# Performance work log

Measured on AMD Instinct MI355X. Metric: run time of the kernel, lower is better.

The kernel has to match this reference:

```python
import jax, jax.numpy as jnp
import numpy as np

N = 10000       # nodes
E = 320000      # edges (before self-loops)
IN = 128
HID = 256
OUT = 256
HEADS = 4
C = HID // HEADS  # 64 per-head channels
NEG_SLOPE = 0.2   # PyG GATConv default
BN_EPS = 1e-5


def setup_inputs() -> dict:
    key = jax.random.key(0)
    ks = jax.random.split(key, 24)
    x = jax.random.normal(ks[0], (N, IN), jnp.float32)
    edge_index = jax.random.randint(ks[1], (2, E), 0, N, dtype=jnp.int64)

    def glorot(k, shape, fan_in):
        return jax.random.normal(k, shape, jnp.float32) * (1.0 / np.sqrt(fan_in))

    inp = {"x": x, "edge_index": edge_index}
    # layer 0: IN -> HEADS x C (concat)
    inp["W0"] = glorot(ks[2], (IN, HEADS * C), IN)
    inp["as0"] = glorot(ks[3], (HEADS, C), C)
    inp["ad0"] = glorot(ks[4], (HEADS, C), C)
    inp["b0"] = jnp.zeros((HEADS * C,), jnp.float32)
    inp["g0"] = jnp.ones((HID,), jnp.float32)
    inp["be0"] = jnp.zeros((HID,), jnp.float32)
    # layer 1: HID -> HEADS x C (concat)
    inp["W1"] = glorot(ks[5], (HID, HEADS * C), HID)
    inp["as1"] = glorot(ks[6], (HEADS, C), C)
    inp["ad1"] = glorot(ks[7], (HEADS, C), C)
    inp["b1"] = jnp.zeros((HEADS * C,), jnp.float32)
    inp["g1"] = jnp.ones((HID,), jnp.float32)
    inp["be1"] = jnp.zeros((HID,), jnp.float32)
    # layer 2: HID -> OUT, heads=1, concat=False
    inp["W2"] = glorot(ks[8], (HID, OUT), HID)
    inp["as2"] = glorot(ks[9], (1, OUT), OUT)
    inp["ad2"] = glorot(ks[10], (1, OUT), OUT)
    inp["b2"] = jnp.zeros((OUT,), jnp.float32)
    inp["g2"] = jnp.ones((OUT,), jnp.float32)
    inp["be2"] = jnp.zeros((OUT,), jnp.float32)
    return inp


def gat_conv(x, src, dst, W, att_src, att_dst, bias, concat):
    """PyG GATConv (add_self_loops already applied to src/dst)."""
    H, Ch = att_src.shape
    h = (x @ W).reshape(-1, H, Ch)                      # [N, H, C]
    a_src = jnp.einsum('nhc,hc->nh', h, att_src)        # [N, H]
    a_dst = jnp.einsum('nhc,hc->nh', h, att_dst)
    alpha = jax.nn.leaky_relu(a_src[src] + a_dst[dst], NEG_SLOPE)  # [E', H]
    # segment softmax over incoming edges of each dst node
    amax = jax.ops.segment_max(alpha, dst, num_segments=N)
    alpha = jnp.exp(alpha - amax[dst])
    denom = jax.ops.segment_sum(alpha, dst, num_segments=N)
    alpha = alpha / (denom[dst] + 1e-16)
    msg = h[src] * alpha[:, :, None]                    # [E', H, C]
    out = jax.ops.segment_sum(msg, dst, num_segments=N) # [N, H, C]
    out = out.reshape(N, H * Ch) if concat else out.mean(axis=1)
    return out + bias


def batch_norm(x, gamma, beta):
    # training-mode BatchNorm1d over node dim (biased variance, eps=1e-5)
    m = x.mean(axis=0)
    v = jnp.mean((x - m) ** 2, axis=0)
    return (x - m) * jax.lax.rsqrt(v + BN_EPS) * gamma + beta


def reference(x, edge_index,
              W0, as0, ad0, b0, g0, be0,
              W1, as1, ad1, b1, g1, be1,
              W2, as2, ad2, b2, g2, be2):
    loop = jnp.arange(N, dtype=edge_index.dtype)
    src = jnp.concatenate([edge_index[0], loop])
    dst = jnp.concatenate([edge_index[1], loop])

    h = gat_conv(x, src, dst, W0, as0, ad0, b0, concat=True)
    h = jax.nn.relu(batch_norm(h, g0, be0))  # dropout inactive in eval
    h = gat_conv(h, src, dst, W1, as1, ad1, b1, concat=True)
    h = jax.nn.relu(batch_norm(h, g1, be1))
    h = gat_conv(h, src, dst, W2, as2, ad2, b2, concat=False)
    h = batch_norm(h, g2, be2)
    return h
```

## Files before the change

### kernel.cpp

```cpp
#include <hip/hip_runtime.h>
#include <math.h>

#define NN 10000
#define EE 320000
#define ET (EE + NN)

typedef __attribute__((ext_vector_type(8))) short short8;
typedef __attribute__((ext_vector_type(4))) float f32x4;
typedef unsigned short u16;

static __device__ __forceinline__ float b2f(u16 u) {
  return __uint_as_float(((unsigned)u) << 16);
}
static __device__ __forceinline__ u16 f2b(float f) {
  unsigned u = __float_as_uint(f);
  unsigned r = (u + 0x7FFFu + ((u >> 16) & 1u)) >> 16;
  return (u16)r;
}

__global__ void k_count(const int* __restrict__ ei, int* __restrict__ cnt) {
  int e = blockIdx.x * 256 + threadIdx.x;
  if (e < EE) atomicAdd(&cnt[ei[EE + e]], 1);
}

__global__ __launch_bounds__(1024) void k_scan(const int* __restrict__ cnt,
                                               int* __restrict__ rowst,
                                               int* __restrict__ cursor,
                                               int* __restrict__ csrc) {
  __shared__ int ws[16];
  int tid = threadIdx.x, lane = tid & 63, wv = tid >> 6;
  int base = tid * 10;
  int v[10];
  int tot = 0;
#pragma unroll
  for (int i = 0; i < 10; i++) {
    int idx = base + i;
    v[i] = (idx < NN) ? (cnt[idx] + 1) : 0;
    tot += v[i];
  }
  int sc = tot;
#pragma unroll
  for (int off = 1; off < 64; off <<= 1) {
    int t = __shfl_up(sc, off);
    if (lane >= off) sc += t;
  }
  if (lane == 63) ws[wv] = sc;
  __syncthreads();
  if (wv == 0 && lane < 16) {
    int val = ws[lane];
    int s = val;
#pragma unroll
    for (int off = 1; off < 16; off <<= 1) {
      int t = __shfl_up(s, off);
      if (lane >= off) s += t;
    }
    ws[lane] = s - val;
  }
  __syncthreads();
  int run = ws[wv] + sc - tot;
#pragma unroll
  for (int i = 0; i < 10; i++) {
    int idx = base + i;
    if (idx < NN) {
      rowst[idx] = run;
      csrc[run] = idx;
      cursor[idx] = run + 1;
      run += v[i];
    }
  }
  if (tid == 1023) rowst[NN] = run;
}

__global__ void k_fill(const int* __restrict__ ei, int* __restrict__ cursor,
                       int* __restrict__ csrc) {
  int e = blockIdx.x * 256 + threadIdx.x;
  if (e < EE) {
    int d = ei[EE + e];
    int pos = atomicAdd(&cursor[d], 1);
    csrc[pos] = ei[e];
  }
}

__global__ void k_casts(const float* __restrict__ x, const float* __restrict__ W0,
                        const float* __restrict__ W1, const float* __restrict__ W2,
                        u16* __restrict__ abf, u16* __restrict__ Wt0,
                        u16* __restrict__ Wt1, u16* __restrict__ Wt2) {
  int t = blockIdx.x * 256 + threadIdx.x;
  const int NX4 = NN * 128 / 4;
  if (t < NX4) {
    float4 f = ((const float4*)x)[t];
    ushort4 o;
    o.x = f2b(f.x); o.y = f2b(f.y); o.z = f2b(f.z); o.w = f2b(f.w);
    ((ushort4*)abf)[t] = o;
    return;
  }
  int u = t - NX4;
  if (u < 128 * 256) {
    int nI = u / 128, k = u - nI * 128;
    Wt0[u] = f2b(W0[(size_t)k * 256 + nI]);
    return;
  }
  u -= 128 * 256;
  if (u < 256 * 256) {
    int nI = u / 256, k = u - nI * 256;
    Wt1[u] = f2b(W1[(size_t)k * 256 + nI]);
    return;
  }
  u -= 256 * 256;
  if (u < 256 * 256) {
    int nI = u / 256, k = u - nI * 256;
    Wt2[u] = f2b(W2[(size_t)k * 256 + nI]);
  }
}

template <int KK, int BN>
__global__ __launch_bounds__(256) void k_gemm(
    const u16* __restrict__ A, const float* __restrict__ Af,
    const float* __restrict__ bkt, const float* __restrict__ gam,
    const float* __restrict__ bet, const u16* __restrict__ Wt,
    const float* __restrict__ as, const float* __restrict__ ad,
    u16* __restrict__ hb, float* __restrict__ asrc, float* __restrict__ adst,
    int H) {
  __shared__ float2 bnp[256];
  if (BN) {
    int t = threadIdx.x;
    float s = 0.f, q = 0.f;
#pragma unroll 8
    for (int b = 0; b < 32; b++) {
      s += bkt[b * 512 + t];
      q += bkt[b * 512 + 256 + t];
    }
    float m = s * (1.0f / NN);
    float v = q * (1.0f / NN) - m * m;
    float rs = rsqrtf(v + 1e-5f) * gam[t];
    bnp[t] = make_float2(rs, bet[t] - m * rs);
    __syncthreads();
  }
  int wv = threadIdx.x >> 6, lane = threadIdx.x & 63;
  int row0 = blockIdx.x * 64 + wv * 16;
  int col0 = blockIdx.y * 128;
  int r = lane & 15, g = lane >> 4;
  f32x4 acc[8];
#pragma unroll
  for (int nt = 0; nt < 8; nt++) acc[nt] = (f32x4){0.f, 0.f, 0.f, 0.f};

  int ar = row0 + r;
  if (ar > NN - 1) ar = NN - 1;

#pragma unroll
  for (int ks = 0; ks < KK / 32; ks++) {
    short8 af;
    if (BN == 0) {
      af = *(const short8*)(A + (size_t)ar * KK + ks * 32 + g * 8);
    } else {
      int c0 = ks * 32 + g * 8;
      float4 a0 = ((const float4*)Af)[(size_t)ar * (KK / 4) + c0 / 4];
      float4 a1 = ((const float4*)Af)[(size_t)ar * (KK / 4) + c0 / 4 + 1];
      float vv[8] = {a0.x, a0.y, a0.z, a0.w, a1.x, a1.y, a1.z, a1.w};
#pragma unroll
      for (int j = 0; j < 8; j++) {
        float2 p = bnp[c0 + j];
        float t = fmaxf(fmaf(vv[j], p.x, p.y), 0.f);
        af[j] = (short)f2b(t);
      }
    }
#pragma unroll
    for (int nt = 0; nt < 8; nt++) {
      short8 bf = *(const short8*)(Wt + (size_t)(col0 + nt * 16 + r) * KK + ks * 32 + g * 8);
      acc[nt] = __builtin_amdgcn_mfma_f32_16x16x32_bf16(af, bf, acc[nt], 0, 0, 0);
    }
  }
#pragma unroll
  for (int nt = 0; nt < 8; nt++) {
    int col = col0 + nt * 16 + r;
#pragma unroll
    for (int q = 0; q < 4; q++) {
      int row = row0 + g * 4 + q;
      if (row < NN) hb[(size_t)row * 256 + col] = f2b(acc[nt][q]);
    }
  }
  float asv[8], adv[8];
#pragma unroll
  for (int nt = 0; nt < 8; nt++) {
    asv[nt] = as[col0 + nt * 16 + r];
    adv[nt] = ad[col0 + nt * 16 + r];
  }
#pragma unroll
  for (int q = 0; q < 4; q++) {
    int row = row0 + g * 4 + q;
    if (H == 4) {
#pragma unroll
      for (int hh = 0; hh < 2; hh++) {
        float ps = 0.f, pd = 0.f;
#pragma unroll
        for (int k = 0; k < 4; k++) {
          ps = fmaf(acc[hh * 4 + k][q], asv[hh * 4 + k], ps);
          pd = fmaf(acc[hh * 4 + k][q], adv[hh * 4 + k], pd);
        }
#pragma unroll
        for (int off = 1; off < 16; off <<= 1) {
          ps += __shfl_xor(ps, off);
          pd += __shfl_xor(pd, off);
        }
        if (r == 0 && row < NN) {
          int slot = 2 * blockIdx.y + hh;
          asrc[row * 4 + slot] = ps;
          adst[row * 4 + slot] = pd;
        }
      }
    } else {
      float ps = 0.f, pd = 0.f;
#pragma unroll
      for (int nt = 0; nt < 8; nt++) {
        ps = fmaf(acc[nt][q], asv[nt], ps);
        pd = fmaf(acc[nt][q], adv[nt], pd);
      }
#pragma unroll
      for (int off = 1; off < 16; off <<= 1) {
        ps += __shfl_xor(ps, off);
        pd += __shfl_xor(pd, off);
      }
      if (r == 0 && row < NN) {
        int slot = 2 * blockIdx.y;
        asrc[row * 4 + slot] = ps;
        asrc[row * 4 + slot + 1] = 0.f;
        adst[row * 4 + slot] = pd;
        adst[row * 4 + slot + 1] = 0.f;
      }
    }
  }
}

template <int H>
__global__ __launch_bounds__(256) void k_softagg(
    const int* __restrict__ rowst, const int* __restrict__ csrc,
    const float* __restrict__ asrc, const float* __restrict__ adst,
    const u16* __restrict__ hb, const float* __restrict__ bias,
    float* __restrict__ out, float* __restrict__ bkt) {
  __shared__ int lds_s[4][128];
  __shared__ float lds_w[4][128][H];
  __shared__ float4 lds_rv[4][64];
  __shared__ float4 lds_rq[4][64];
  int wv = threadIdx.x >> 6, lane = threadIdx.x & 63;
  int n = blockIdx.x * 4 + wv;
  int rs = rowst[n], re = rowst[n + 1];

  float ad[H];
  {
    float4 t = ((const float4*)adst)[n];
    if (H == 4) { ad[0] = t.x; ad[1] = t.y; ad[2] = t.z; ad[3] = t.w; }
    else ad[0] = t.x + t.y + t.z + t.w;
  }
  float mx[H], sm[H];
#pragma unroll
  for (int h = 0; h < H; h++) { mx[h] = -1e30f; sm[h] = 0.f; }

  int e0 = rs + lane, e1 = e0 + 64;
  bool h0 = e0 < re, h1 = e1 < re;
  float a0[H], a1[H];

  if (h0) {
    int s = csrc[e0];
    lds_s[wv][lane] = s;
    float4 t = ((const float4*)asrc)[s];
    if (H == 4) { a0[0] = t.x; a0[1] = t.y; a0[2] = t.z; a0[3] = t.w; }
    else a0[0] = t.x + t.y + t.z + t.w;
#pragma unroll
    for (int h = 0; h < H; h++) {
      float v = a0[h] + ad[h];
      v = v > 0.f ? v : 0.2f * v;
      a0[h] = v;
      mx[h] = fmaxf(mx[h], v);
    }
  }
  if (h1) {
    int s = csrc[e1];
    lds_s[wv][64 + lane] = s;
    float4 t = ((const float4*)asrc)[s];
    if (H == 4) { a1[0] = t.x; a1[1] = t.y; a1[2] = t.z; a1[3] = t.w; }
    else a1[0] = t.x + t.y + t.z + t.w;
#pragma unroll
    for (int h = 0; h < H; h++) {
      float v = a1[h] + ad[h];
      v = v > 0.f ? v : 0.2f * v;
      a1[h] = v;
      mx[h] = fmaxf(mx[h], v);
    }
  }
  for (int e = rs + 128 + lane; e < re; e += 64) {
    int s = csrc[e];
    float4 t = ((const float4*)asrc)[s];
    float a[H];
    if (H == 4) { a[0] = t.x; a[1] = t.y; a[2] = t.z; a[3] = t.w; }
    else a[0] = t.x + t.y + t.z + t.w;
#pragma unroll
    for (int h = 0; h < H; h++) {
      float v = a[h] + ad[h];
      v = v > 0.f ? v : 0.2f * v;
      mx[h] = fmaxf(mx[h], v);
    }
  }
#pragma unroll
  for (int off = 32; off; off >>= 1)
#pragma unroll
    for (int h = 0; h < H; h++) mx[h] = fmaxf(mx[h], __shfl_xor(mx[h], off));

  if (h0) {
#pragma unroll
    for (int h = 0; h < H; h++) {
      a0[h] = __expf(a0[h] - mx[h]);
      sm[h] += a0[h];
      lds_w[wv][lane][h] = a0[h];
    }
  }
  if (h1) {
#pragma unroll
    for (int h = 0; h < H; h++) {
      a1[h] = __expf(a1[h] - mx[h]);
      sm[h] += a1[h];
      lds_w[wv][64 + lane][h] = a1[h];
    }
  }
  for (int e = rs + 128 + lane; e < re; e += 64) {
    int s = csrc[e];
    float4 t = ((const float4*)asrc)[s];
    float a[H];
    if (H == 4) { a[0] = t.x; a[1] = t.y; a[2] = t.z; a[3] = t.w; }
    else a[0] = t.x + t.y + t.z + t.w;
#pragma unroll
    for (int h = 0; h < H; h++) {
      float v = a[h] + ad[h];
      v = v > 0.f ? v : 0.2f * v;
      sm[h] += __expf(v - mx[h]);
    }
  }
#pragma unroll
  for (int off = 32; off; off >>= 1)
#pragma unroll
    for (int h = 0; h < H; h++) sm[h] += __shfl_xor(sm[h], off);

  float inv[H];
#pragma unroll
  for (int h = 0; h < H; h++) inv[h] = 1.0f / (sm[h] + 1e-16f);

  __syncthreads();

  int hd = (H == 4) ? (lane >> 4) : 0;
  const ushort4* h4 = (const ushort4*)hb;
  float4 A0 = {0.f, 0.f, 0.f, 0.f}, A1 = {0.f, 0.f, 0.f, 0.f};
  int m = re - rs;
  if (m > 128) m = 128;
  int e = 0;
  for (; e + 8 <= m; e += 8) {
    int ss[8];
    float ww[8];
    ushort4 v[8];
#pragma unroll
    for (int j = 0; j < 8; j++) ss[j] = lds_s[wv][e + j];
#pragma unroll
    for (int j = 0; j < 8; j++) ww[j] = lds_w[wv][e + j][hd];
#pragma unroll
    for (int j = 0; j < 8; j++) v[j] = h4[(size_t)ss[j] * 64 + lane];
#pragma unroll
    for (int j = 0; j < 8; j++) {
      float w = ww[j];
      if (j & 1) {
        A1.x = fmaf(w, b2f(v[j].x), A1.x);
        A1.y = fmaf(w, b2f(v[j].y), A1.y);
        A1.z = fmaf(w, b2f(v[j].z), A1.z);
        A1.w = fmaf(w, b2f(v[j].w), A1.w);
      } else {
        A0.x = fmaf(w, b2f(v[j].x), A0.x);
        A0.y = fmaf(w, b2f(v[j].y), A0.y);
        A0.z = fmaf(w, b2f(v[j].z), A0.z);
        A0.w = fmaf(w, b2f(v[j].w), A0.w);
      }
    }
  }
  for (; e < m; e++) {
    int s = lds_s[wv][e];
    float w = lds_w[wv][e][hd];
    ushort4 v = h4[(size_t)s * 64 + lane];
    A0.x = fmaf(w, b2f(v.x), A0.x);
    A0.y = fmaf(w, b2f(v.y), A0.y);
    A0.z = fmaf(w, b2f(v.z), A0.z);
    A0.w = fmaf(w, b2f(v.w), A0.w);
  }
  for (int ee = rs + 128; ee < re; ee++) {
    int s = csrc[ee];
    float4 t = ((const float4*)asrc)[s];
    float av, adh, mh;
    if (H == 4) {
      av = hd == 0 ? t.x : hd == 1 ? t.y : hd == 2 ? t.z : t.w;
      adh = hd == 0 ? ad[0] : hd == 1 ? ad[1] : hd == 2 ? ad[2] : ad[3];
      mh = hd == 0 ? mx[0] : hd == 1 ? mx[1] : hd == 2 ? mx[2] : mx[3];
    } else {
      av = t.x + t.y + t.z + t.w;
      adh = ad[0];
      mh = mx[0];
    }
    float vv = av + adh;
    vv = vv > 0.f ? vv : 0.2f * vv;
    float w = __expf(vv - mh);
    ushort4 v = h4[(size_t)s * 64 + lane];
    A0.x = fmaf(w, b2f(v.x), A0.x);
    A0.y = fmaf(w, b2f(v.y), A0.y);
    A0.z = fmaf(w, b2f(v.z), A0.z);
    A0.w = fmaf(w, b2f(v.w), A0.w);
  }
  float invh;
  if (H == 4)
    invh = hd == 0 ? inv[0] : hd == 1 ? inv[1] : hd == 2 ? inv[2] : inv[3];
  else
    invh = inv[0];
  float4 b4 = ((const float4*)bias)[lane];
  float4 r4;
  r4.x = (A0.x + A1.x) * invh + b4.x;
  r4.y = (A0.y + A1.y) * invh + b4.y;
  r4.z = (A0.z + A1.z) * invh + b4.z;
  r4.w = (A0.w + A1.w) * invh + b4.w;
  ((float4*)out)[(size_t)n * 64 + lane] = r4;

  float4 q4;
  q4.x = r4.x * r4.x; q4.y = r4.y * r4.y;
  q4.z = r4.z * r4.z; q4.w = r4.w * r4.w;
  lds_rv[wv][lane] = r4;
  lds_rq[wv][lane] = q4;
  __syncthreads();
  if (wv == 0) {
    float4 sv = lds_rv[0][lane], sq = lds_rq[0][lane];
#pragma unroll
    for (int w = 1; w < 4; w++) {
      float4 tv = lds_rv[w][lane], tq = lds_rq[w][lane];
      sv.x += tv.x; sv.y += tv.y; sv.z += tv.z; sv.w += tv.w;
      sq.x += tq.x; sq.y += tq.y; sq.z += tq.z; sq.w += tq.w;
    }
    float* pv = bkt + (blockIdx.x & 31) * 512 + lane * 4;
    atomicAdd(pv + 0, sv.x); atomicAdd(pv + 1, sv.y);
    atomicAdd(pv + 2, sv.z); atomicAdd(pv + 3, sv.w);
    float* pq = pv + 256;
    atomicAdd(pq + 0, sq.x); atomicAdd(pq + 1, sq.y);
    atomicAdd(pq + 2, sq.z); atomicAdd(pq + 3, sq.w);
  }
}

__global__ void k_bnred(const float* __restrict__ bkt, const float* __restrict__ g,
                        const float* __restrict__ be, float* __restrict__ rsg,
                        float* __restrict__ sh) {
  int t = threadIdx.x;
  float s = 0.f, q = 0.f;
#pragma unroll 8
  for (int b = 0; b < 32; b++) {
    s += bkt[b * 512 + t];
    q += bkt[b * 512 + 256 + t];
  }
  float m = s * (1.0f / NN);
  float v = q * (1.0f / NN) - m * m;
  float rs = rsqrtf(v + 1e-5f) * g[t];
  rsg[t] = rs;
  sh[t] = be[t] - m * rs;
}

__global__ void k_bnout(const float* __restrict__ x, const float* __restrict__ rsg,
                        const float* __restrict__ sh, float* __restrict__ y) {
  int i = blockIdx.x * 256 + threadIdx.x;
  int c = i & 63;
  float4 rs4 = ((const float4*)rsg)[c];
  float4 sh4 = ((const float4*)sh)[c];
  float4 xv = ((const float4*)x)[i];
  float4 r;
  r.x = fmaf(xv.x, rs4.x, sh4.x);
  r.y = fmaf(xv.y, rs4.y, sh4.y);
  r.z = fmaf(xv.z, rs4.z, sh4.z);
  r.w = fmaf(xv.w, rs4.w, sh4.w);
  ((float4*)y)[i] = r;
}

extern "C" void kernel_launch(void* const* d_in, const int* in_sizes, int n_in,
                              void* d_out, int out_size, void* d_ws, size_t ws_size,
                              hipStream_t stream) {
  const float* x   = (const float*)d_in[0];
  const int*   ei  = (const int*)d_in[1];
  const float* W0  = (const float*)d_in[2];
  const float* as0 = (const float*)d_in[3];
  const float* ad0 = (const float*)d_in[4];
  const float* b0  = (const float*)d_in[5];
  const float* g0  = (const float*)d_in[6];
  const float* be0 = (const float*)d_in[7];
  const float* W1  = (const float*)d_in[8];
  const float* as1 = (const float*)d_in[9];
  const float* ad1 = (const float*)d_in[10];
  const float* b1  = (const float*)d_in[11];
  const float* g1  = (const float*)d_in[12];
  const float* be1 = (const float*)d_in[13];
  const float* W2  = (const float*)d_in[14];
  const float* as2 = (const float*)d_in[15];
  const float* ad2 = (const float*)d_in[16];
  const float* b2  = (const float*)d_in[17];
  const float* g2  = (const float*)d_in[18];
  const float* be2 = (const float*)d_in[19];
  float* out = (float*)d_out;

  u16* hb  = (u16*)d_ws;
  u16* abf = hb + (size_t)NN * 256;
  u16* Wt0 = abf + (size_t)NN * 128;
  u16* Wt1 = Wt0 + 256 * 128;
  u16* Wt2 = Wt1 + 256 * 256;
  float* asrc = (float*)(Wt2 + 256 * 256);
  float* adst = asrc + NN * 4;
  float* aggf = adst + NN * 4;
  float* bkt  = aggf + (size_t)NN * 256;
  float* rsg2 = bkt + 3 * 32 * 512;
  float* sh2  = rsg2 + 256;
  int* cnt    = (int*)(sh2 + 256);
  int* rowst  = cnt + NN;
  int* cursor = rowst + NN + 1;
  int* csrc   = cursor + NN;

  hipMemsetAsync(bkt, 0, (3 * 32 * 512 + 512 + NN) * sizeof(float), stream);
  k_count<<<(EE + 255) / 256, 256, 0, stream>>>(ei, cnt);
  k_scan<<<1, 1024, 0, stream>>>(cnt, rowst, cursor, csrc);
  k_fill<<<(EE + 255) / 256, 256, 0, stream>>>(ei, cursor, csrc);
  {
    int total = NN * 128 / 4 + 128 * 256 + 256 * 256 + 256 * 256;
    k_casts<<<(total + 255) / 256, 256, 0, stream>>>(x, W0, W1, W2, abf, Wt0, Wt1, Wt2);
  }

  dim3 ggrid((NN + 63) / 64, 2);

  k_gemm<128, 0><<<ggrid, 256, 0, stream>>>(abf, nullptr, nullptr, nullptr, nullptr,
                                            Wt0, as0, ad0, hb, asrc, adst, 4);
  k_softagg<4><<<NN / 4, 256, 0, stream>>>(rowst, csrc, asrc, adst, hb, b0, aggf, bkt);

  k_gemm<256, 1><<<ggrid, 256, 0, stream>>>(nullptr, aggf, bkt, g0, be0,
                                            Wt1, as1, ad1, hb, asrc, adst, 4);
  k_softagg<4><<<NN / 4, 256, 0, stream>>>(rowst, csrc, asrc, adst, hb, b1, aggf,
                                           bkt + 32 * 512);

  k_gemm<256, 1><<<ggrid, 256, 0, stream>>>(nullptr, aggf, bkt + 32 * 512, g1, be1,
                                            Wt2, as2, ad2, hb, asrc, adst, 1);
  k_softagg<1><<<NN / 4, 256, 0, stream>>>(rowst, csrc, asrc, adst, hb, b2, aggf,
                                           bkt + 2 * 32 * 512);

  k_bnred<<<1, 256, 0, stream>>>(bkt + 2 * 32 * 512, g2, be2, rsg2, sh2);
  k_bnout<<<NN / 4, 256, 0, stream>>>(aggf, rsg2, sh2, out);
}
```

Before: 338.0 us.

## Store intermediate activations as bf16, widen aggregation loads, and merge count and cast kernels

The softmax-aggregation kernel now writes the hidden layers' output as bf16 instead of fp32. The following GEMM reads that bf16 buffer directly, which halves activation traffic between the stages. The aggregation loop is restructured so each wave processes two edges per step with 16-byte gathers: edges are padded to a multiple of 16 with zero weights, and the two halves are combined with a shuffle. The BN statistics reduction now uses all 256 threads for the atomics, and the edge-count and cast kernels are merged to save a launch. BN statistics are computed from the fp32 values before rounding, while the next layer consumes bf16-rounded values, which adds a small precision loss.

```diff
diff --git a/kernel.cpp b/kernel.cpp
--- a/kernel.cpp
+++ b/kernel.cpp
@@ -6,6 +6,7 @@
 #define ET (EE + NN)
 
 typedef __attribute__((ext_vector_type(8))) short short8;
+typedef __attribute__((ext_vector_type(8))) unsigned short ushort8_t;
 typedef __attribute__((ext_vector_type(4))) float f32x4;
 typedef unsigned short u16;
 
@@ -18,9 +19,38 @@
   return (u16)r;
 }
 
-__global__ void k_count(const int* __restrict__ ei, int* __restrict__ cnt) {
-  int e = blockIdx.x * 256 + threadIdx.x;
-  if (e < EE) atomicAdd(&cnt[ei[EE + e]], 1);
+__global__ void k_castcnt(const int* __restrict__ ei, int* __restrict__ cnt,
+                          const float* __restrict__ x, const float* __restrict__ W0,
+                          const float* __restrict__ W1, const float* __restrict__ W2,
+                          u16* __restrict__ abf, u16* __restrict__ Wt0,
+                          u16* __restrict__ Wt1, u16* __restrict__ Wt2) {
+  int t = blockIdx.x * 256 + threadIdx.x;
+  if (t < EE) atomicAdd(&cnt[ei[EE + t]], 1);
+  const int NX4 = NN * 128 / 4;
+  if (t < NX4) {
+    float4 f = ((const float4*)x)[t];
+    ushort4 o;
+    o.x = f2b(f.x); o.y = f2b(f.y); o.z = f2b(f.z); o.w = f2b(f.w);
+    ((ushort4*)abf)[t] = o;
+    return;
+  }
+  int u = t - NX4;
+  if (u < 128 * 256) {
+    int nI = u / 128, k = u - nI * 128;
+    Wt0[u] = f2b(W0[(size_t)k * 256 + nI]);
+    return;
+  }
+  u -= 128 * 256;
+  if (u < 256 * 256) {
+    int nI = u / 256, k = u - nI * 256;
+    Wt1[u] = f2b(W1[(size_t)k * 256 + nI]);
+    return;
+  }
+  u -= 256 * 256;
+  if (u < 256 * 256) {
+    int nI = u / 256, k = u - nI * 256;
+    Wt2[u] = f2b(W2[(size_t)k * 256 + nI]);
+  }
 }
 
 __global__ __launch_bounds__(1024) void k_scan(const int* __restrict__ cnt,
@@ -81,46 +111,13 @@
   }
 }
 
-__global__ void k_casts(const float* __restrict__ x, const float* __restrict__ W0,
-                        const float* __restrict__ W1, const float* __restrict__ W2,
-                        u16* __restrict__ abf, u16* __restrict__ Wt0,
-                        u16* __restrict__ Wt1, u16* __restrict__ Wt2) {
-  int t = blockIdx.x * 256 + threadIdx.x;
-  const int NX4 = NN * 128 / 4;
-  if (t < NX4) {
-    float4 f = ((const float4*)x)[t];
-    ushort4 o;
-    o.x = f2b(f.x); o.y = f2b(f.y); o.z = f2b(f.z); o.w = f2b(f.w);
-    ((ushort4*)abf)[t] = o;
-    return;
-  }
-  int u = t - NX4;
-  if (u < 128 * 256) {
-    int nI = u / 128, k = u - nI * 128;
-    Wt0[u] = f2b(W0[(size_t)k * 256 + nI]);
-    return;
-  }
-  u -= 128 * 256;
-  if (u < 256 * 256) {
-    int nI = u / 256, k = u - nI * 256;
-    Wt1[u] = f2b(W1[(size_t)k * 256 + nI]);
-    return;
-  }
-  u -= 256 * 256;
-  if (u < 256 * 256) {
-    int nI = u / 256, k = u - nI * 256;
-    Wt2[u] = f2b(W2[(size_t)k * 256 + nI]);
-  }
-}
-
 template <int KK, int BN>
 __global__ __launch_bounds__(256) void k_gemm(
-    const u16* __restrict__ A, const float* __restrict__ Af,
-    const float* __restrict__ bkt, const float* __restrict__ gam,
-    const float* __restrict__ bet, const u16* __restrict__ Wt,
-    const float* __restrict__ as, const float* __restrict__ ad,
-    u16* __restrict__ hb, float* __restrict__ asrc, float* __restrict__ adst,
-    int H) {
+    const u16* __restrict__ A, const float* __restrict__ bkt,
+    const float* __restrict__ gam, const float* __restrict__ bet,
+    const u16* __restrict__ Wt, const float* __restrict__ as,
+    const float* __restrict__ ad, u16* __restrict__ hb,
+    float* __restrict__ asrc, float* __restrict__ adst, int H) {
   __shared__ float2 bnp[256];
   if (BN) {
     int t = threadIdx.x;
@@ -150,17 +147,15 @@
 #pragma unroll
   for (int ks = 0; ks < KK / 32; ks++) {
     short8 af;
+    short8 raw = *(const short8*)(A + (size_t)ar * KK + ks * 32 + g * 8);
     if (BN == 0) {
-      af = *(const short8*)(A + (size_t)ar * KK + ks * 32 + g * 8);
+      af = raw;
     } else {
       int c0 = ks * 32 + g * 8;
-      float4 a0 = ((const float4*)Af)[(size_t)ar * (KK / 4) + c0 / 4];
-      float4 a1 = ((const float4*)Af)[(size_t)ar * (KK / 4) + c0 / 4 + 1];
-      float vv[8] = {a0.x, a0.y, a0.z, a0.w, a1.x, a1.y, a1.z, a1.w};
 #pragma unroll
       for (int j = 0; j < 8; j++) {
         float2 p = bnp[c0 + j];
-        float t = fmaxf(fmaf(vv[j], p.x, p.y), 0.f);
+        float t = fmaxf(fmaf(b2f((u16)raw[j]), p.x, p.y), 0.f);
         af[j] = (short)f2b(t);
       }
     }
@@ -231,16 +226,16 @@
   }
 }
 
-template <int H>
+template <int H, int BOUT>
 __global__ __launch_bounds__(256) void k_softagg(
     const int* __restrict__ rowst, const int* __restrict__ csrc,
     const float* __restrict__ asrc, const float* __restrict__ adst,
     const u16* __restrict__ hb, const float* __restrict__ bias,
-    float* __restrict__ out, float* __restrict__ bkt) {
+    float* __restrict__ outf, u16* __restrict__ outb, float* __restrict__ bkt) {
   __shared__ int lds_s[4][128];
   __shared__ float lds_w[4][128][H];
-  __shared__ float4 lds_rv[4][64];
-  __shared__ float4 lds_rq[4][64];
+  __shared__ float lds_v[4][256];
+  __shared__ float lds_q[4][256];
   int wv = threadIdx.x >> 6, lane = threadIdx.x & 63;
   int n = blockIdx.x * 4 + wv;
   int rs = rowst[n], re = rowst[n + 1];
@@ -343,105 +338,88 @@
 #pragma unroll
   for (int h = 0; h < H; h++) inv[h] = 1.0f / (sm[h] + 1e-16f);
 
-  __syncthreads();
-
-  int hd = (H == 4) ? (lane >> 4) : 0;
-  const ushort4* h4 = (const ushort4*)hb;
-  float4 A0 = {0.f, 0.f, 0.f, 0.f}, A1 = {0.f, 0.f, 0.f, 0.f};
   int m = re - rs;
   if (m > 128) m = 128;
-  int e = 0;
-  for (; e + 8 <= m; e += 8) {
+  int mp = (m + 15) & ~15;
+  for (int p = m + lane; p < mp; p += 64) {
+    lds_s[wv][p] = n;
+#pragma unroll
+    for (int h = 0; h < H; h++) lds_w[wv][p][h] = 0.f;
+  }
+
+  int cl = lane & 31, half = lane >> 5;
+  int hd8 = (H == 4) ? (cl >> 3) : 0;
+  float invh = (H == 4) ? (hd8 == 0 ? inv[0] : hd8 == 1 ? inv[1] : hd8 == 2 ? inv[2] : inv[3])
+                        : inv[0];
+  float mh = (H == 4) ? (hd8 == 0 ? mx[0] : hd8 == 1 ? mx[1] : hd8 == 2 ? mx[2] : mx[3])
+                      : mx[0];
+  float adh = (H == 4) ? (hd8 == 0 ? ad[0] : hd8 == 1 ? ad[1] : hd8 == 2 ? ad[2] : ad[3])
+                       : ad[0];
+  const ushort8_t* h8 = (const ushort8_t*)hb;
+  float acc[8] = {0.f, 0.f, 0.f, 0.f, 0.f, 0.f, 0.f, 0.f};
+  for (int e = 0; e < mp; e += 16) {
     int ss[8];
     float ww[8];
-    ushort4 v[8];
-#pragma unroll
-    for (int j = 0; j < 8; j++) ss[j] = lds_s[wv][e + j];
-#pragma unroll
-    for (int j = 0; j < 8; j++) ww[j] = lds_w[wv][e + j][hd];
-#pragma unroll
-    for (int j = 0; j < 8; j++) v[j] = h4[(size_t)ss[j] * 64 + lane];
-#pragma unroll
-    for (int j = 0; j < 8; j++) {
-      float w = ww[j];
-      if (j & 1) {
-        A1.x = fmaf(w, b2f(v[j].x), A1.x);
-        A1.y = fmaf(w, b2f(v[j].y), A1.y);
-        A1.z = fmaf(w, b2f(v[j].z), A1.z);
-        A1.w = fmaf(w, b2f(v[j].w), A1.w);
-      } else {
-        A0.x = fmaf(w, b2f(v[j].x), A0.x);
-        A0.y = fmaf(w, b2f(v[j].y), A0.y);
-        A0.z = fmaf(w, b2f(v[j].z), A0.z);
-        A0.w = fmaf(w, b2f(v[j].w), A0.w);
-      }
-    }
-  }
-  for (; e < m; e++) {
-    int s = lds_s[wv][e];
-    float w = lds_w[wv][e][hd];
-    ushort4 v = h4[(size_t)s * 64 + lane];
-    A0.x = fmaf(w, b2f(v.x), A0.x);
-    A0.y = fmaf(w, b2f(v.y), A0.y);
-    A0.z = fmaf(w, b2f(v.z), A0.z);
-    A0.w = fmaf(w, b2f(v.w), A0.w);
-  }
-  for (int ee = rs + 128; ee < re; ee++) {
+    ushort8_t vv[8];
+#pragma unroll
+    for (int j = 0; j < 8; j++) ss[j] = lds_s[wv][e + 2 * j + half];
+#pragma unroll
+    for (int j = 0; j < 8; j++) ww[j] = lds_w[wv][e + 2 * j + half][hd8];
+#pragma unroll
+    for (int j = 0; j < 8; j++) vv[j] = h8[(size_t)ss[j] * 32 + cl];
+#pragma unroll
+    for (int j = 0; j < 8; j++)
+#pragma unroll
+      for (int k = 0; k < 8; k++) acc[k] = fmaf(ww[j], b2f((u16)vv[j][k]), acc[k]);
+  }
+  for (int ee = rs + 128 + half; ee < re; ee += 2) {
     int s = csrc[ee];
     float4 t = ((const float4*)asrc)[s];
-    float av, adh, mh;
-    if (H == 4) {
-      av = hd == 0 ? t.x : hd == 1 ? t.y : hd == 2 ? t.z : t.w;
-      adh = hd == 0 ? ad[0] : hd == 1 ? ad[1] : hd == 2 ? ad[2] : ad[3];
-      mh = hd == 0 ? mx[0] : hd == 1 ? mx[1] : hd == 2 ? mx[2] : mx[3];
+    float av = (H == 4) ? (hd8 == 0 ? t.x : hd8 == 1 ? t.y : hd8 == 2 ? t.z : t.w)
+                        : (t.x + t.y + t.z + t.w);
+    float vv2 = av + adh;
+    vv2 = vv2 > 0.f ? vv2 : 0.2f * vv2;
+    float w = __expf(vv2 - mh);
+    ushort8_t v = h8[(size_t)s * 32 + cl];
+#pragma unroll
+    for (int k = 0; k < 8; k++) acc[k] = fmaf(w, b2f((u16)v[k]), acc[k]);
+  }
+#pragma unroll
+  for (int k = 0; k < 8; k++) acc[k] += __shfl_xor(acc[k], 32);
+
+  float4 ba = ((const float4*)bias)[cl * 2];
+  float4 bb = ((const float4*)bias)[cl * 2 + 1];
+  float r8[8];
+  r8[0] = acc[0] * invh + ba.x; r8[1] = acc[1] * invh + ba.y;
+  r8[2] = acc[2] * invh + ba.z; r8[3] = acc[3] * invh + ba.w;
+  r8[4] = acc[4] * invh + bb.x; r8[5] = acc[5] * invh + bb.y;
+  r8[6] = acc[6] * invh + bb.z; r8[7] = acc[7] * invh + bb.w;
+
+  if (half == 0) {
+    if (BOUT) {
+      ushort8_t o;
+#pragma unroll
+      for (int k = 0; k < 8; k++) o[k] = f2b(r8[k]);
+      ((ushort8_t*)outb)[(size_t)n * 32 + cl] = o;
     } else {
-      av = t.x + t.y + t.z + t.w;
-      adh = ad[0];
-      mh = mx[0];
-    }
-    float vv = av + adh;
-    vv = vv > 0.f ? vv : 0.2f * vv;
-    float w = __expf(vv - mh);
-    ushort4 v = h4[(size_t)s * 64 + lane];
-    A0.x = fmaf(w, b2f(v.x), A0.x);
-    A0.y = fmaf(w, b2f(v.y), A0.y);
-    A0.z = fmaf(w, b2f(v.z), A0.z);
-    A0.w = fmaf(w, b2f(v.w), A0.w);
-  }
-  float invh;
-  if (H == 4)
-    invh = hd == 0 ? inv[0] : hd == 1 ? inv[1] : hd == 2 ? inv[2] : inv[3];
-  else
-    invh = inv[0];
-  float4 b4 = ((const float4*)bias)[lane];
-  float4 r4;
-  r4.x = (A0.x + A1.x) * invh + b4.x;
-  r4.y = (A0.y + A1.y) * invh + b4.y;
-  r4.z = (A0.z + A1.z) * invh + b4.z;
-  r4.w = (A0.w + A1.w) * invh + b4.w;
-  ((float4*)out)[(size_t)n * 64 + lane] = r4;
-
-  float4 q4;
-  q4.x = r4.x * r4.x; q4.y = r4.y * r4.y;
-  q4.z = r4.z * r4.z; q4.w = r4.w * r4.w;
-  lds_rv[wv][lane] = r4;
-  lds_rq[wv][lane] = q4;
+      float4 w0 = make_float4(r8[0], r8[1], r8[2], r8[3]);
+      float4 w1 = make_float4(r8[4], r8[5], r8[6], r8[7]);
+      ((float4*)outf)[(size_t)n * 64 + cl * 2] = w0;
+      ((float4*)outf)[(size_t)n * 64 + cl * 2 + 1] = w1;
+    }
+#pragma unroll
+    for (int k = 0; k < 8; k++) {
+      lds_v[wv][cl * 8 + k] = r8[k];
+      lds_q[wv][cl * 8 + k] = r8[k] * r8[k];
+    }
+  }
   __syncthreads();
-  if (wv == 0) {
-    float4 sv = lds_rv[0][lane], sq = lds_rq[0][lane];
-#pragma unroll
-    for (int w = 1; w < 4; w++) {
-      float4 tv = lds_rv[w][lane], tq = lds_rq[w][lane];
-      sv.x += tv.x; sv.y += tv.y; sv.z += tv.z; sv.w += tv.w;
-      sq.x += tq.x; sq.y += tq.y; sq.z += tq.z; sq.w += tq.w;
-    }
-    float* pv = bkt + (blockIdx.x & 31) * 512 + lane * 4;
-    atomicAdd(pv + 0, sv.x); atomicAdd(pv + 1, sv.y);
-    atomicAdd(pv + 2, sv.z); atomicAdd(pv + 3, sv.w);
-    float* pq = pv + 256;
-    atomicAdd(pq + 0, sq.x); atomicAdd(pq + 1, sq.y);
-    atomicAdd(pq + 2, sq.z); atomicAdd(pq + 3, sq.w);
-  }
+  int t = threadIdx.x;
+  float sv = lds_v[0][t] + lds_v[1][t] + lds_v[2][t] + lds_v[3][t];
+  float sq = lds_q[0][t] + lds_q[1][t] + lds_q[2][t] + lds_q[3][t];
+  float* pv = bkt + (blockIdx.x & 31) * 512;
+  atomicAdd(pv + t, sv);
+  atomicAdd(pv + 256 + t, sq);
 }
 
 __global__ void k_bnred(const float* __restrict__ bkt, const float* __restrict__ g,
@@ -501,11 +479,12 @@
   const float* be2 = (const float*)d_in[19];
   float* out = (float*)d_out;
 
-  u16* hb  = (u16*)d_ws;
-  u16* abf = hb + (size_t)NN * 256;
-  u16* Wt0 = abf + (size_t)NN * 128;
-  u16* Wt1 = Wt0 + 256 * 128;
-  u16* Wt2 = Wt1 + 256 * 256;
+  u16* hb   = (u16*)d_ws;
+  u16* abf  = hb + (size_t)NN * 256;
+  u16* ab16 = abf + (size_t)NN * 128;
+  u16* Wt0  = ab16 + (size_t)NN * 256;
+  u16* Wt1  = Wt0 + 256 * 128;
+  u16* Wt2  = Wt1 + 256 * 256;
   float* asrc = (float*)(Wt2 + 256 * 256);
   float* adst = asrc + NN * 4;
   float* aggf = adst + NN * 4;
@@ -518,29 +497,30 @@
   int* csrc   = cursor + NN;
 
   hipMemsetAsync(bkt, 0, (3 * 32 * 512 + 512 + NN) * sizeof(float), stream);
-  k_count<<<(EE + 255) / 256, 256, 0, stream>>>(ei, cnt);
+  {
+    int total = NN * 128 / 4 + 128 * 256 + 256 * 256 + 256 * 256;
+    k_castcnt<<<(total + 255) / 256, 256, 0, stream>>>(ei, cnt, x, W0, W1, W2,
+                                                       abf, Wt0, Wt1, Wt2);
+  }
   k_scan<<<1, 1024, 0, stream>>>(cnt, rowst, cursor, csrc);
   k_fill<<<(EE + 255) / 256, 256, 0, stream>>>(ei, cursor, csrc);
-  {
-    int total = NN * 128 / 4 + 128 * 256 + 256 * 256 + 256 * 256;
-    k_casts<<<(total + 255) / 256, 256, 0, stream>>>(x, W0, W1, W2, abf, Wt0, Wt1, Wt2);
-  }
 
   dim3 ggrid((NN + 63) / 64, 2);
 
-  k_gemm<128, 0><<<ggrid, 256, 0, stream>>>(abf, nullptr, nullptr, nullptr, nullptr,
+  k_gemm<128, 0><<<ggrid, 256, 0, stream>>>(abf, nullptr, nullptr, nullptr,
                                             Wt0, as0, ad0, hb, asrc, adst, 4);
-  k_softagg<4><<<NN / 4, 256, 0, stream>>>(rowst, csrc, asrc, adst, hb, b0, aggf, bkt);
-
-  k_gemm<256, 1><<<ggrid, 256, 0, stream>>>(nullptr, aggf, bkt, g0, be0,
+  k_softagg<4, 1><<<NN / 4, 256, 0, stream>>>(rowst, csrc, asrc, adst, hb, b0,
+                                              nullptr, ab16, bkt);
+
+  k_gemm<256, 1><<<ggrid, 256, 0, stream>>>(ab16, bkt, g0, be0,
                                             Wt1, as1, ad1, hb, asrc, adst, 4);
-  k_softagg<4><<<NN / 4, 256, 0, stream>>>(rowst, csrc, asrc, adst, hb, b1, aggf,
-                                           bkt + 32 * 512);
-
-  k_gemm<256, 1><<<ggrid, 256, 0, stream>>>(nullptr, aggf, bkt + 32 * 512, g1, be1,
+  k_softagg<4, 1><<<NN / 4, 256, 0, stream>>>(rowst, csrc, asrc, adst, hb, b1,
+                                              nullptr, ab16, bkt + 32 * 512);
+
+  k_gemm<256, 1><<<ggrid, 256, 0, stream>>>(ab16, bkt + 32 * 512, g1, be1,
                                             Wt2, as2, ad2, hb, asrc, adst, 1);
-  k_softagg<1><<<NN / 4, 256, 0, stream>>>(rowst, csrc, asrc, adst, hb, b2, aggf,
-                                           bkt + 2 * 32 * 512);
+  k_softagg<1, 0><<<NN / 4, 256, 0, stream>>>(rowst, csrc, asrc, adst, hb, b2,
+                                              aggf, nullptr, bkt + 2 * 32 * 512);
 
   k_bnred<<<1, 256, 0, stream>>>(bkt + 2 * 32 * 512, g2, be2, rsg2, sh2);
   k_bnout<<<NN / 4, 256, 0, stream>>>(aggf, rsg2, sh2, out);
```

Result: faster. 293.1 us (-13.3%).
